# Kernel tuning notes

Hardware: AMD Instinct MI355X
Metric: run time of the kernel (lower is better)

Reference implementation:

```python
import jax, jax.numpy as jnp
import numpy as np

B, A, T, NH, NEMB = 8, 32, 64, 256, 256
E = A * (A - 1)  # fully-connected directed edges, no self-loops


def _onehot_edges():
    # NRI-style: rows of off-diagonal pairs (send i -> recv j, i != j)
    send_idx, recv_idx = [], []
    for i in range(A):
        for j in range(A):
            if i != j:
                send_idx.append(i)
                recv_idx.append(j)
    rel_send = jax.nn.one_hot(jnp.array(send_idx), A, dtype=jnp.float32)
    rel_rec = jax.nn.one_hot(jnp.array(recv_idx), A, dtype=jnp.float32)
    return rel_rec, rel_send


def setup_inputs() -> dict:
    key = jax.random.key(0)
    k1, k2, k3 = jax.random.split(key, 3)
    h = jax.random.normal(k1, (B, A, T, NH), dtype=jnp.float32)
    rel_rec, rel_send = _onehot_edges()
    # nn.Linear(2*n_h, n_emb): W [n_emb, 2*n_h], b [n_emb]
    lim = 1.0 / np.sqrt(2 * NH)
    W = jax.random.uniform(k2, (NEMB, 2 * NH), minval=-lim, maxval=lim, dtype=jnp.float32)
    b = jax.random.uniform(k3, (NEMB,), minval=-lim, maxval=lim, dtype=jnp.float32)
    return {"h": h, "rel_rec": rel_rec, "rel_send": rel_send, "W": W, "b": b}


def reference(h, rel_rec, rel_send, W, b):
    # h: [B, A, T, NH]; rel_rec/rel_send: [E, A] one-hot selectors
    # Equivalent to reshape->batched matmul->reshape in the torch code,
    # expressed as a single contraction over atoms.
    receivers = jnp.einsum('ea,bath->beth', rel_rec, h)   # [B, E, T, NH]
    senders = jnp.einsum('ea,bath->beth', rel_send, h)    # [B, E, T, NH]
    edges = jnp.concatenate([senders, receivers], axis=-1)  # [B, E, T, 2*NH]
    return jnp.einsum('betf,of->beto', edges, W) + b        # [B, E, T, NEMB]
```

## Files before the change

### kernel.cpp

```cpp
#include <hip/hip_runtime.h>
#include <hip/hip_bf16.h>

using f32x4  = __attribute__((ext_vector_type(4))) float;
using bf16x8 = __attribute__((ext_vector_type(8))) short;
using s16x4  = __attribute__((ext_vector_type(4))) short;

constexpr int kB  = 8;
constexpr int kA  = 32;
constexpr int kT  = 64;
constexpr int kNH = 256;
constexpr int kNE = 256;
constexpr int kE  = kA * (kA - 1);
constexpr int kM  = kB * kA * kT;
constexpr int kK  = kNH;
constexpr int kN  = 2 * kNE;

__device__ __forceinline__ unsigned short rne_bf16(float f) {
    unsigned int u = __float_as_uint(f);
    u += 0x7fffu + ((u >> 16) & 1u);
    return (unsigned short)(u >> 16);
}
__device__ __forceinline__ float bf16_f32(unsigned short h) {
    return __uint_as_float(((unsigned int)h) << 16);
}
__device__ __forceinline__ void split2(float x, unsigned short& h, unsigned short& m) {
    h = rne_bf16(x);
    float r1 = x - bf16_f32(h);
    m = rne_bf16(r1);
}

#define GLL(g, l) __builtin_amdgcn_global_load_lds( \
    (const __attribute__((address_space(1))) void*)(g), \
    (__attribute__((address_space(3))) void*)(l), 16, 0, 0)

#define FLAG_ADD(slot) __hip_atomic_fetch_add(&flags[(slot) * 16], 1u, \
    __ATOMIC_RELAXED, __HIP_MEMORY_SCOPE_AGENT)
#define FLAG_WAIT(slot, tgt)                                                   \
    while (__hip_atomic_load(&flags[(slot) * 16], __ATOMIC_RELAXED,            \
                             __HIP_MEMORY_SCOPE_AGENT) < (unsigned)(tgt))      \
        __builtin_amdgcn_s_sleep(1)

__global__ __launch_bounds__(256, 2) void k_all(const float* __restrict__ hsrc,
                                                const float* __restrict__ W,
                                                const float* __restrict__ rel_rec,
                                                const float* __restrict__ rel_send,
                                                const float* __restrict__ bias,
                                                unsigned short* __restrict__ a1,
                                                unsigned short* __restrict__ a2,
                                                unsigned short* __restrict__ b1,
                                                unsigned short* __restrict__ b2,
                                                float* __restrict__ P,
                                                int* __restrict__ ij2e,
                                                unsigned int* flags,
                                                float* __restrict__ out) {
    __shared__ unsigned short sAh[128 * 32], sAm[128 * 32];
    __shared__ unsigned short sBh[128 * 32], sBm[128 * 32];

    const int bid = blockIdx.x;
    const int tid = threadIdx.x;
    const int xcd = bid & 7;
    const int idx = bid >> 3;
    const int bn  = idx & 3;
    const int bm  = xcd * 16 + (idx >> 2);

    unsigned short* b1x = b1 + (size_t)xcd * (kN * kK);
    unsigned short* b2x = b2 + (size_t)xcd * (kN * kK);
    int*            lut = ij2e + xcd * 1024;

    {
        const int row0 = bm * 128 + bn * 32;
        const size_t base4 = (size_t)row0 * 64;
#pragma unroll
        for (int r = 0; r < 8; ++r) {
            size_t i4 = base4 + (size_t)r * 256 + tid;
            f32x4 v = ((const f32x4*)hsrc)[i4];
            s16x4 o1, o2;
#pragma unroll
            for (int j = 0; j < 4; ++j) {
                unsigned short h, m;
                split2(v[j], h, m);
                o1[j] = (short)h; o2[j] = (short)m;
            }
            *(s16x4*)(a1 + i4 * 4) = o1;
            *(s16x4*)(a2 + i4 * 4) = o2;
        }
#pragma unroll
        for (int r = 0; r < 8; ++r) {
            int n = idx * 8 + r;
            float wv = (n < kNE) ? W[(size_t)n * (2 * kNH) + tid]
                                 : W[(size_t)(n - kNE) * (2 * kNH) + kNH + tid];
            unsigned short wh, wm;
            split2(wv, wh, wm);
            b1x[(size_t)n * kK + tid] = wh;
            b2x[(size_t)n * kK + tid] = wm;
        }
        if (idx < 4) {
            int e = idx * 256 + tid;
            if (e < kE) {
                int ir = 0, is = 0;
                for (int a = 0; a < kA; ++a) {
                    if (rel_rec[(size_t)e * kA + a]  > 0.5f) ir = a;
                    if (rel_send[(size_t)e * kA + a] > 0.5f) is = a;
                }
                lut[is * kA + ir] = e;
            }
        }
        __syncthreads();
        if (tid == 0) {
            FLAG_ADD(bm);
            FLAG_ADD(256 + xcd);
            if (idx < 4) FLAG_ADD(264 + xcd);
        }
    }

    {
        if (tid == 0) { FLAG_WAIT(bm, 4); FLAG_WAIT(256 + xcd, 64); }
        __syncthreads();
        asm volatile("" ::: "memory");

        const int lane = tid & 63;
        const int wave = tid >> 6;
        const int wr = wave >> 1, wc = wave & 1;

        const int sr   = tid >> 2;
        const int scb  = (tid & 3) << 4;
        const int scbs = scb ^ (((sr >> 1) & 3) << 4);
        const size_t rA  = (size_t)(bm * 128 + sr) * kK + (scbs >> 1);
        const size_t rB  = (size_t)(bn * 128 + sr) * kK + (scbs >> 1);
        const size_t rA1 = rA + (size_t)64 * kK;
        const size_t rB1 = rB + (size_t)64 * kK;
        const int l0 = tid * 8, l1 = 64 * 32 + tid * 8;

        const int fr  = lane & 15;
        const int fkb = (lane >> 4) << 4;
        const int swz = ((fr >> 1) & 3) << 4;

        f32x4 acc[4][4] = {};

#pragma unroll
        for (int kt = 0; kt < 8; ++kt) {
            const int kk = kt * 32;
            __syncthreads();
            GLL(a1  + rA + kk, sAh + l0);  GLL(a1  + rA1 + kk, sAh + l1);
            GLL(a2  + rA + kk, sAm + l0);  GLL(a2  + rA1 + kk, sAm + l1);
            GLL(b1x + rB + kk, sBh + l0);  GLL(b1x + rB1 + kk, sBh + l1);
            GLL(b2x + rB + kk, sBm + l0);  GLL(b2x + rB1 + kk, sBm + l1);
            __syncthreads();

            bf16x8 ah[4], am[4], bh[4], bmf[4];
#pragma unroll
            for (int mi = 0; mi < 4; ++mi) {
                int row = wr * 64 + mi * 16 + fr;
                int off = row * 64 + (fkb ^ swz);
                ah[mi] = *(const bf16x8*)((const char*)sAh + off);
                am[mi] = *(const bf16x8*)((const char*)sAm + off);
            }
#pragma unroll
            for (int ni = 0; ni < 4; ++ni) {
                int row = wc * 64 + ni * 16 + fr;
                int off = row * 64 + (fkb ^ swz);
                bh[ni]  = *(const bf16x8*)((const char*)sBh + off);
                bmf[ni] = *(const bf16x8*)((const char*)sBm + off);
            }
#pragma unroll
            for (int mi = 0; mi < 4; ++mi)
#pragma unroll
                for (int ni = 0; ni < 4; ++ni) {
                    f32x4 c = acc[mi][ni];
                    c = __builtin_amdgcn_mfma_f32_16x16x32_bf16(ah[mi], bh[ni],  c, 0, 0, 0);
                    c = __builtin_amdgcn_mfma_f32_16x16x32_bf16(ah[mi], bmf[ni], c, 0, 0, 0);
                    c = __builtin_amdgcn_mfma_f32_16x16x32_bf16(am[mi], bh[ni],  c, 0, 0, 0);
                    acc[mi][ni] = c;
                }
        }

        const int col = lane & 15;
        const int rb  = (lane >> 4) << 2;
#pragma unroll
        for (int mi = 0; mi < 4; ++mi)
#pragma unroll
            for (int ni = 0; ni < 4; ++ni) {
                int n = bn * 128 + wc * 64 + ni * 16 + col;
#pragma unroll
                for (int r = 0; r < 4; ++r) {
                    int m = bm * 128 + wr * 64 + mi * 16 + rb + r;
                    P[(size_t)m * kN + n] = acc[mi][ni][r];
                }
            }
        __syncthreads();
        if (tid == 0) FLAG_ADD(128 + bm);
    }

    {
        const int b  = xcd;
        const int gi = (bid >> 3) & 7;
        const int gj = (bid >> 6) & 7;
        const int m0 = b * 16 + 2 * gi;
        const int m2 = b * 16 + 2 * gj;
        if (tid == 0) {
            FLAG_WAIT(264 + xcd, 4);
            FLAG_WAIT(128 + m0, 4);  FLAG_WAIT(128 + m0 + 1, 4);
            FLAG_WAIT(128 + m2, 4);  FLAG_WAIT(128 + m2 + 1, 4);
        }
        __syncthreads();
        asm volatile("" ::: "memory");

        int* se = (int*)sAh;
        if (tid < 16) {
            int si = tid >> 2, rj = tid & 3;
            int i = gi * 4 + si, j = gj * 4 + rj;
            se[tid] = (i == j) ? -1 : lut[i * kA + j];
        }
        __syncthreads();
        int e[16];
#pragma unroll
        for (int k = 0; k < 16; ++k) e[k] = se[k];

        const int c = tid & 63;
        const int w = tid >> 6;
        f32x4 bv = ((const f32x4*)bias)[c];
        const float* Pb = P + (size_t)(b * kA) * kT * kN;
        float* outb = out + (size_t)b * kE * kT * kNE;

        for (int i = 0; i < 16; ++i) {
            int t = w + i * 4;
            f32x4 ps[4], pr[4];
#pragma unroll
            for (int si = 0; si < 4; ++si)
                ps[si] = *(const f32x4*)(Pb + ((size_t)(gi * 4 + si) * kT + t) * kN + c * 4);
#pragma unroll
            for (int rj = 0; rj < 4; ++rj)
                pr[rj] = *(const f32x4*)(Pb + ((size_t)(gj * 4 + rj) * kT + t) * kN + kNE + c * 4);
#pragma unroll
            for (int si = 0; si < 4; ++si)
#pragma unroll
                for (int rj = 0; rj < 4; ++rj) {
                    int ee = e[si * 4 + rj];
                    if (ee >= 0) {
                        f32x4 v = ps[si] + pr[rj] + bv;
                        __builtin_nontemporal_store(
                            v, (f32x4*)(outb + ((size_t)ee * kT + t) * kNE + c * 4));
                    }
                }
        }
    }
}

extern "C" void kernel_launch(void* const* d_in, const int* in_sizes, int n_in,
                              void* d_out, int out_size, void* d_ws, size_t ws_size,
                              hipStream_t stream) {
    const float* h    = (const float*)d_in[0];
    const float* rrec = (const float*)d_in[1];
    const float* rsnd = (const float*)d_in[2];
    const float* W    = (const float*)d_in[3];
    const float* bias = (const float*)d_in[4];
    float* out = (float*)d_out;

    char* ws = (char*)d_ws;
    const size_t MB = 1024 * 1024;
    unsigned short* Ah = (unsigned short*)(ws);
    unsigned short* Am = (unsigned short*)(ws + 8 * MB);
    unsigned short* Bh = (unsigned short*)(ws + 16 * MB);
    unsigned short* Bm = (unsigned short*)(ws + 18 * MB);
    float* P   = (float*)(ws + 20 * MB);
    int* ij2e  = (int*)(ws + 52 * MB);
    unsigned int* flags = (unsigned int*)(ws + 52 * MB + 64 * 1024);

    hipMemsetAsync(flags, 0, 32 * 1024, stream);
    k_all<<<dim3(512), dim3(256), 0, stream>>>(h, W, rrec, rsnd, bias,
                                               Ah, Am, Bh, Bm, P, ij2e, flags, out);
}
```

Before: 129.7 us.

## Split blocks into dedicated GEMM and scatter roles with larger per-block work

```diff
diff --git a/kernel.cpp b/kernel.cpp
--- a/kernel.cpp
+++ b/kernel.cpp
@@ -60,15 +60,15 @@
     const int tid = threadIdx.x;
     const int xcd = bid & 7;
     const int idx = bid >> 3;
-    const int bn  = idx & 3;
-    const int bm  = xcd * 16 + (idx >> 2);
 
     unsigned short* b1x = b1 + (size_t)xcd * (kN * kK);
     unsigned short* b2x = b2 + (size_t)xcd * (kN * kK);
     int*            lut = ij2e + xcd * 1024;
 
     {
-        const int row0 = bm * 128 + bn * 32;
+        const int sbn = idx & 3;
+        const int sbm = xcd * 16 + (idx >> 2);
+        const int row0 = sbm * 128 + sbn * 32;
         const size_t base4 = (size_t)row0 * 64;
 #pragma unroll
         for (int r = 0; r < 8; ++r) {
@@ -107,13 +107,17 @@
         }
         __syncthreads();
         if (tid == 0) {
-            FLAG_ADD(bm);
+            FLAG_ADD(sbm);
             FLAG_ADD(256 + xcd);
             if (idx < 4) FLAG_ADD(264 + xcd);
         }
     }
 
-    {
+    if (bid < 256) {
+        const int j  = idx;
+        const int bm = xcd * 16 + (j >> 1);
+        const int bn0 = (j & 1) * 2;
+
         if (tid == 0) { FLAG_WAIT(bm, 4); FLAG_WAIT(256 + xcd, 64); }
         __syncthreads();
         asm volatile("" ::: "memory");
@@ -126,95 +130,98 @@
         const int scb  = (tid & 3) << 4;
         const int scbs = scb ^ (((sr >> 1) & 3) << 4);
         const size_t rA  = (size_t)(bm * 128 + sr) * kK + (scbs >> 1);
-        const size_t rB  = (size_t)(bn * 128 + sr) * kK + (scbs >> 1);
         const size_t rA1 = rA + (size_t)64 * kK;
-        const size_t rB1 = rB + (size_t)64 * kK;
         const int l0 = tid * 8, l1 = 64 * 32 + tid * 8;
 
         const int fr  = lane & 15;
         const int fkb = (lane >> 4) << 4;
         const int swz = ((fr >> 1) & 3) << 4;
-
-        f32x4 acc[4][4] = {};
-
-#pragma unroll
-        for (int kt = 0; kt < 8; ++kt) {
-            const int kk = kt * 32;
-            __syncthreads();
-            GLL(a1  + rA + kk, sAh + l0);  GLL(a1  + rA1 + kk, sAh + l1);
-            GLL(a2  + rA + kk, sAm + l0);  GLL(a2  + rA1 + kk, sAm + l1);
-            GLL(b1x + rB + kk, sBh + l0);  GLL(b1x + rB1 + kk, sBh + l1);
-            GLL(b2x + rB + kk, sBm + l0);  GLL(b2x + rB1 + kk, sBm + l1);
-            __syncthreads();
-
-            bf16x8 ah[4], am[4], bh[4], bmf[4];
-#pragma unroll
-            for (int mi = 0; mi < 4; ++mi) {
-                int row = wr * 64 + mi * 16 + fr;
-                int off = row * 64 + (fkb ^ swz);
-                ah[mi] = *(const bf16x8*)((const char*)sAh + off);
-                am[mi] = *(const bf16x8*)((const char*)sAm + off);
-            }
-#pragma unroll
-            for (int ni = 0; ni < 4; ++ni) {
-                int row = wc * 64 + ni * 16 + fr;
-                int off = row * 64 + (fkb ^ swz);
-                bh[ni]  = *(const bf16x8*)((const char*)sBh + off);
-                bmf[ni] = *(const bf16x8*)((const char*)sBm + off);
-            }
-#pragma unroll
-            for (int mi = 0; mi < 4; ++mi)
-#pragma unroll
-                for (int ni = 0; ni < 4; ++ni) {
-                    f32x4 c = acc[mi][ni];
-                    c = __builtin_amdgcn_mfma_f32_16x16x32_bf16(ah[mi], bh[ni],  c, 0, 0, 0);
-                    c = __builtin_amdgcn_mfma_f32_16x16x32_bf16(ah[mi], bmf[ni], c, 0, 0, 0);
-                    c = __builtin_amdgcn_mfma_f32_16x16x32_bf16(am[mi], bh[ni],  c, 0, 0, 0);
-                    acc[mi][ni] = c;
-                }
-        }
-
         const int col = lane & 15;
         const int rb  = (lane >> 4) << 2;
-#pragma unroll
-        for (int mi = 0; mi < 4; ++mi)
-#pragma unroll
-            for (int ni = 0; ni < 4; ++ni) {
-                int n = bn * 128 + wc * 64 + ni * 16 + col;
-#pragma unroll
-                for (int r = 0; r < 4; ++r) {
-                    int m = bm * 128 + wr * 64 + mi * 16 + rb + r;
-                    P[(size_t)m * kN + n] = acc[mi][ni][r];
-                }
+
+        for (int tn = 0; tn < 2; ++tn) {
+            const int bn = bn0 + tn;
+            const size_t rB  = (size_t)(bn * 128 + sr) * kK + (scbs >> 1);
+            const size_t rB1 = rB + (size_t)64 * kK;
+
+            f32x4 acc[4][4] = {};
+#pragma unroll
+            for (int kt = 0; kt < 8; ++kt) {
+                const int kk = kt * 32;
+                __syncthreads();
+                GLL(a1  + rA + kk, sAh + l0);  GLL(a1  + rA1 + kk, sAh + l1);
+                GLL(a2  + rA + kk, sAm + l0);  GLL(a2  + rA1 + kk, sAm + l1);
+                GLL(b1x + rB + kk, sBh + l0);  GLL(b1x + rB1 + kk, sBh + l1);
+                GLL(b2x + rB + kk, sBm + l0);  GLL(b2x + rB1 + kk, sBm + l1);
+                __syncthreads();
+
+                bf16x8 ah[4], am[4], bh[4], bmf[4];
+#pragma unroll
+                for (int mi = 0; mi < 4; ++mi) {
+                    int row = wr * 64 + mi * 16 + fr;
+                    int off = row * 64 + (fkb ^ swz);
+                    ah[mi] = *(const bf16x8*)((const char*)sAh + off);
+                    am[mi] = *(const bf16x8*)((const char*)sAm + off);
+                }
+#pragma unroll
+                for (int ni = 0; ni < 4; ++ni) {
+                    int row = wc * 64 + ni * 16 + fr;
+                    int off = row * 64 + (fkb ^ swz);
+                    bh[ni]  = *(const bf16x8*)((const char*)sBh + off);
+                    bmf[ni] = *(const bf16x8*)((const char*)sBm + off);
+                }
+#pragma unroll
+                for (int mi = 0; mi < 4; ++mi)
+#pragma unroll
+                    for (int ni = 0; ni < 4; ++ni) {
+                        f32x4 c = acc[mi][ni];
+                        c = __builtin_amdgcn_mfma_f32_16x16x32_bf16(ah[mi], bh[ni],  c, 0, 0, 0);
+                        c = __builtin_amdgcn_mfma_f32_16x16x32_bf16(ah[mi], bmf[ni], c, 0, 0, 0);
+                        c = __builtin_amdgcn_mfma_f32_16x16x32_bf16(am[mi], bh[ni],  c, 0, 0, 0);
+                        acc[mi][ni] = c;
+                    }
             }
-        __syncthreads();
-        if (tid == 0) FLAG_ADD(128 + bm);
-    }
-
-    {
-        const int b  = xcd;
-        const int gi = (bid >> 3) & 7;
-        const int gj = (bid >> 6) & 7;
-        const int m0 = b * 16 + 2 * gi;
-        const int m2 = b * 16 + 2 * gj;
+
+#pragma unroll
+            for (int mi = 0; mi < 4; ++mi)
+#pragma unroll
+                for (int ni = 0; ni < 4; ++ni) {
+                    int n = bn * 128 + wc * 64 + ni * 16 + col;
+#pragma unroll
+                    for (int r = 0; r < 4; ++r) {
+                        int m = bm * 128 + wr * 64 + mi * 16 + rb + r;
+                        P[(size_t)m * kN + n] = acc[mi][ni][r];
+                    }
+                }
+            __syncthreads();
+            if (tid == 0) FLAG_ADD(128 + bm);
+        }
+    } else {
+        const int j   = idx - 32;
+        const int b   = xcd;
+        const int gi  = j >> 2;
+        const int gj0 = (2 * j) & 7;
+        const int ms = b * 16 + 2 * gi;
+        const int mr = b * 16 + 2 * gj0;
         if (tid == 0) {
             FLAG_WAIT(264 + xcd, 4);
-            FLAG_WAIT(128 + m0, 4);  FLAG_WAIT(128 + m0 + 1, 4);
-            FLAG_WAIT(128 + m2, 4);  FLAG_WAIT(128 + m2 + 1, 4);
+            FLAG_WAIT(128 + ms, 4);      FLAG_WAIT(128 + ms + 1, 4);
+            FLAG_WAIT(128 + mr, 4);      FLAG_WAIT(128 + mr + 1, 4);
+            FLAG_WAIT(128 + mr + 2, 4);  FLAG_WAIT(128 + mr + 3, 4);
         }
         __syncthreads();
         asm volatile("" ::: "memory");
 
         int* se = (int*)sAh;
-        if (tid < 16) {
-            int si = tid >> 2, rj = tid & 3;
-            int i = gi * 4 + si, j = gj * 4 + rj;
-            se[tid] = (i == j) ? -1 : lut[i * kA + j];
-        }
-        __syncthreads();
-        int e[16];
-#pragma unroll
-        for (int k = 0; k < 16; ++k) e[k] = se[k];
+        if (tid < 32) {
+            int si = tid >> 3, rj = tid & 7;
+            int i = gi * 4 + si, jj = gj0 * 4 + rj;
+            se[tid] = (i == jj) ? -1 : lut[i * kA + jj];
+        }
+        __syncthreads();
+        int e[32];
+#pragma unroll
+        for (int k = 0; k < 32; ++k) e[k] = se[k];
 
         const int c = tid & 63;
         const int w = tid >> 6;
@@ -224,18 +231,18 @@
 
         for (int i = 0; i < 16; ++i) {
             int t = w + i * 4;
-            f32x4 ps[4], pr[4];
+            f32x4 ps[4], pr[8];
 #pragma unroll
             for (int si = 0; si < 4; ++si)
                 ps[si] = *(const f32x4*)(Pb + ((size_t)(gi * 4 + si) * kT + t) * kN + c * 4);
 #pragma unroll
-            for (int rj = 0; rj < 4; ++rj)
-                pr[rj] = *(const f32x4*)(Pb + ((size_t)(gj * 4 + rj) * kT + t) * kN + kNE + c * 4);
+            for (int rj = 0; rj < 8; ++rj)
+                pr[rj] = *(const f32x4*)(Pb + ((size_t)(gj0 * 4 + rj) * kT + t) * kN + kNE + c * 4);
 #pragma unroll
             for (int si = 0; si < 4; ++si)
 #pragma unroll
-                for (int rj = 0; rj < 4; ++rj) {
-                    int ee = e[si * 4 + rj];
+                for (int rj = 0; rj < 8; ++rj) {
+                    int ee = e[si * 8 + rj];
                     if (ee >= 0) {
                         f32x4 v = ps[si] + pr[rj] + bv;
                         __builtin_nontemporal_store(
```

Result: slower. 136.8 us (+5.5%).
